# Kernel optimization log

Hardware: AMD Instinct MI355X
Metric: run time of the kernel (lower is better)

Reference implementation:

```python
import jax, jax.numpy as jnp
import numpy as np

N_DOCS = 1_000_000
N_FEAT = 136
BATCH = 1_000_000

# MSLR feature column indices used by the original module
COL_DOCLEN = 14      # metadata docLength
COL_WHOLE_LEN = 16   # used for avgDocLength statistic
COL_TF = 24          # term frequency feature
COL_INLINK = 127
COL_OUTLINK = 128
COL_PAGERANK = 129


def setup_inputs() -> dict:
    key = jax.random.key(0)
    k_feat, k_idx, kb, kpr, kin, kout = jax.random.split(key, 6)
    global_features = jax.random.uniform(k_feat, (N_DOCS, N_FEAT), dtype=jnp.float32)
    batch_indices = jax.random.randint(k_idx, (BATCH,), 0, N_DOCS)
    return {
        "batch_indices": batch_indices,
        "global_features": global_features,
        "k1": jnp.asarray(3.5, jnp.float32),
        "b": jnp.asarray(0.5, jnp.float32),
        "bm25_weight": jnp.asarray(1.0, jnp.float32),
        "page_rank": jnp.asarray(0.2, jnp.float32),
        "in_link": jnp.asarray(0.1, jnp.float32),
        "out_link": jnp.asarray(0.1, jnp.float32),
        "freshness": jnp.asarray(1.0, jnp.float32),
    }


def reference(batch_indices, global_features, k1, b, bm25_weight, page_rank,
              in_link, out_link, freshness):
    # Global doc statistics (computed once, like fetch_total_doc_statistics_mslr)
    avg_doc_len = jnp.mean(global_features[:, COL_WHOLE_LEN])
    total_docs = jnp.float32(global_features.shape[0])

    # Vectorized gather of per-doc features for the batch
    rows = global_features[batch_indices]            # [B, F]
    term_freq = rows[:, COL_TF]                      # [B]
    doc_length = rows[:, COL_DOCLEN]                 # [B]
    pr = rows[:, COL_PAGERANK]
    inl = rows[:, COL_INLINK]
    outl = rows[:, COL_OUTLINK]

    # In the original, num_docs_with_term == total corpus size (constant)
    num_docs_with_term = total_docs
    idf_term = jnp.log((total_docs - num_docs_with_term + 0.5) / (num_docs_with_term + 0.5) + 1.0)

    numerator = term_freq * (k1 + 1.0)
    denominator = term_freq + k1 * (1.0 - b + b * (doc_length / avg_doc_len))
    bm25_score = idf_term * (numerator / denominator)

    pagerank_score = page_rank * pr + in_link * inl + out_link * outl

    # torch.rand(1).item() per doc -> a random constant per doc, scaled by freshness
    fresh_noise = jax.random.uniform(jax.random.key(1), (batch_indices.shape[0],), dtype=jnp.float32)
    freshness_score = fresh_noise * freshness

    scores = bm25_weight * bm25_score + pagerank_score + freshness_score
    return scores[:, None]  # [B, 1]
```

## Files before the change

kernel.cpp:

```cpp
#include <hip/hip_runtime.h>
#include <hip/hip_bf16.h>
#include <stdint.h>

#define N_FEAT 136
#define COL_DOCLEN 14
#define COL_WHOLE_LEN 16
#define COL_TF 24
#define COL_INLINK 127
#define COL_OUTLINK 128
#define COL_PAGERANK 129

__device__ __forceinline__ void threefry2x32(uint32_t k0, uint32_t k1,
                                             uint32_t& x0, uint32_t& x1) {
  const uint32_t ks0 = k0, ks1 = k1, ks2 = k0 ^ k1 ^ 0x1BD11BDAu;
  x0 += ks0; x1 += ks1;
#define TF_ROUND(r) { x0 += x1; x1 = (x1 << (r)) | (x1 >> (32 - (r))); x1 ^= x0; }
  TF_ROUND(13) TF_ROUND(15) TF_ROUND(26) TF_ROUND(6)
  x0 += ks1; x1 += ks2 + 1u;
  TF_ROUND(17) TF_ROUND(29) TF_ROUND(16) TF_ROUND(24)
  x0 += ks2; x1 += ks0 + 2u;
  TF_ROUND(13) TF_ROUND(15) TF_ROUND(26) TF_ROUND(6)
  x0 += ks0; x1 += ks1 + 3u;
  TF_ROUND(17) TF_ROUND(29) TF_ROUND(16) TF_ROUND(24)
  x0 += ks1; x1 += ks2 + 4u;
  TF_ROUND(13) TF_ROUND(15) TF_ROUND(26) TF_ROUND(6)
  x0 += ks2; x1 += ks0 + 5u;
#undef TF_ROUND
}

__global__ void col16_sum_kernel(const float* __restrict__ gf, float* __restrict__ sum,
                                 int n_docs) {
  int stride = gridDim.x * blockDim.x;
  float v = 0.f;
  for (int j = blockIdx.x * blockDim.x + threadIdx.x; j < n_docs; j += stride)
    v += gf[(size_t)j * N_FEAT + COL_WHOLE_LEN];
  for (int off = 32; off > 0; off >>= 1) v += __shfl_down(v, off, 64);
  __shared__ float ws[4];
  int lane = threadIdx.x & 63, wave = threadIdx.x >> 6;
  if (lane == 0) ws[wave] = v;
  __syncthreads();
  if (threadIdx.x == 0) {
    float t = 0.f;
    int nw = blockDim.x >> 6;
    for (int w = 0; w < nw; ++w) t += ws[w];
    atomicAdd(sum, t);
  }
}

__global__ void score_kernel(const int* __restrict__ idx,
                             const float* __restrict__ gf,
                             const float* __restrict__ p_k1,
                             const float* __restrict__ p_b,
                             const float* __restrict__ p_bm25w,
                             const float* __restrict__ p_prw,
                             const float* __restrict__ p_inw,
                             const float* __restrict__ p_outw,
                             const float* __restrict__ p_fresh,
                             const float* __restrict__ col_sum,
                             float* __restrict__ out,
                             int batch, float total_docs) {
  int i = blockIdx.x * blockDim.x + threadIdx.x;
  if (i >= batch) return;

  const float k1 = p_k1[0];
  const float b  = p_b[0];
  const float bm25w = p_bm25w[0];
  const float prw   = p_prw[0];
  const float inw   = p_inw[0];
  const float outw  = p_outw[0];
  const float fresh = p_fresh[0];
  const float avg_doc_len = col_sum[0] / total_docs;

  const float idf = logf(0.5f / (total_docs + 0.5f) + 1.0f);

  const size_t base = (size_t)idx[i] * N_FEAT;
  const float tf   = gf[base + COL_TF];
  const float dl   = gf[base + COL_DOCLEN];
  const float pr   = gf[base + COL_PAGERANK];
  const float inl  = gf[base + COL_INLINK];
  const float outl = gf[base + COL_OUTLINK];

  const float numer = tf * (k1 + 1.0f);
  const float denom = tf + k1 * (1.0f - b + b * (dl / avg_doc_len));
  const float bm25 = idf * (numer / denom);

  uint32_t x0 = 0u, x1 = (uint32_t)i;
  threefry2x32(0u, 1u, x0, x1);
  const uint32_t bits = x0 ^ x1;
  const float noise = __uint_as_float((bits >> 9) | 0x3f800000u) - 1.0f;

  out[i] = bm25w * bm25 + prw * pr + inw * inl + outw * outl + noise * fresh;
}

extern "C" void kernel_launch(void* const* d_in, const int* in_sizes, int n_in,
                              void* d_out, int out_size, void* d_ws, size_t ws_size,
                              hipStream_t stream) {
  const int*   batch_indices = (const int*)d_in[0];
  const float* gf            = (const float*)d_in[1];
  const float* k1    = (const float*)d_in[2];
  const float* b     = (const float*)d_in[3];
  const float* bm25w = (const float*)d_in[4];
  const float* prw   = (const float*)d_in[5];
  const float* inw   = (const float*)d_in[6];
  const float* outw  = (const float*)d_in[7];
  const float* fresh = (const float*)d_in[8];
  float* out = (float*)d_out;
  float* col_sum = (float*)d_ws;

  const int batch  = in_sizes[0];
  const int n_docs = in_sizes[1] / N_FEAT;

  hipMemsetAsync(col_sum, 0, sizeof(float), stream);

  col16_sum_kernel<<<1024, 256, 0, stream>>>(gf, col_sum, n_docs);

  const int threads = 256;
  const int blocks = (batch + threads - 1) / threads;
  score_kernel<<<blocks, threads, 0, stream>>>(
      batch_indices, gf, k1, b, bm25w, prw, inw, outw, fresh,
      col_sum, out, batch, (float)n_docs);
}
```

Baseline: 664.0 us.

## Precompute per-doc scores in a sequential pass, then gather by index

Replaces the random-row gather of five feature columns with a sequential per-document pass. That pass extracts tf, doc length and the link score into compact arrays and computes the column-16 sum at the same time. A second kernel computes a per-document score, and a gather kernel reads one float per batch element with vectorized index loads and stores. The goal is to cut scattered cache-line fetches from the 544-byte rows, though it now touches every document instead of only the sampled ones. It needs workspace for four arrays and falls back to the old path otherwise.

```diff
diff --git a/kernel.cpp b/kernel.cpp
--- a/kernel.cpp
+++ b/kernel.cpp
@@ -1,5 +1,4 @@
 #include <hip/hip_runtime.h>
-#include <hip/hip_bf16.h>
 #include <stdint.h>
 
 #define N_FEAT 136
@@ -28,6 +27,88 @@
 #undef TF_ROUND
 }
 
+__device__ __forceinline__ float tf_noise(uint32_t i) {
+  uint32_t x0 = 0u, x1 = i;
+  threefry2x32(0u, 1u, x0, x1);
+  const uint32_t bits = x0 ^ x1;
+  return __uint_as_float((bits >> 9) | 0x3f800000u) - 1.0f;
+}
+
+__global__ void doc_pass_kernel(const float* __restrict__ gf,
+                                const float* __restrict__ p_prw,
+                                const float* __restrict__ p_inw,
+                                const float* __restrict__ p_outw,
+                                float* __restrict__ tf_a,
+                                float* __restrict__ dl_a,
+                                float* __restrict__ link_a,
+                                float* __restrict__ sum,
+                                int n_docs) {
+  const int j = blockIdx.x * blockDim.x + threadIdx.x;
+  float wl = 0.f;
+  if (j < n_docs) {
+    const size_t base = (size_t)j * N_FEAT;
+    const float dl  = gf[base + COL_DOCLEN];
+    wl              = gf[base + COL_WHOLE_LEN];
+    const float tf  = gf[base + COL_TF];
+    const float inl = gf[base + COL_INLINK];
+    const float2 op = *reinterpret_cast<const float2*>(gf + base + COL_OUTLINK);
+    tf_a[j]   = tf;
+    dl_a[j]   = dl;
+    link_a[j] = p_prw[0] * op.y + p_inw[0] * inl + p_outw[0] * op.x;
+  }
+  for (int off = 32; off > 0; off >>= 1) wl += __shfl_down(wl, off, 64);
+  __shared__ float ws_[4];
+  const int lane = threadIdx.x & 63, wave = threadIdx.x >> 6;
+  if (lane == 0) ws_[wave] = wl;
+  __syncthreads();
+  if (threadIdx.x == 0) atomicAdd(sum, ws_[0] + ws_[1] + ws_[2] + ws_[3]);
+}
+
+__global__ void doc_score_kernel(const float* __restrict__ tf_a,
+                                 const float* __restrict__ dl_a,
+                                 const float* __restrict__ link_a,
+                                 const float* __restrict__ p_k1,
+                                 const float* __restrict__ p_b,
+                                 const float* __restrict__ p_bm25w,
+                                 const float* __restrict__ col_sum,
+                                 float* __restrict__ s_doc,
+                                 int n_docs, float total_docs) {
+  const int j = blockIdx.x * blockDim.x + threadIdx.x;
+  if (j >= n_docs) return;
+  const float k1 = p_k1[0];
+  const float b  = p_b[0];
+  const float bm25w = p_bm25w[0];
+  const float avg_doc_len = col_sum[0] / total_docs;
+  const float idf = logf(0.5f / (total_docs + 0.5f) + 1.0f);
+  const float tf = tf_a[j];
+  const float dl = dl_a[j];
+  const float numer = tf * (k1 + 1.0f);
+  const float denom = tf + k1 * (1.0f - b + b * (dl / avg_doc_len));
+  const float bm25 = idf * (numer / denom);
+  s_doc[j] = bm25w * bm25 + link_a[j];
+}
+
+__global__ void gather_kernel(const int* __restrict__ idx,
+                              const float* __restrict__ s_doc,
+                              const float* __restrict__ p_fresh,
+                              float* __restrict__ out, int batch) {
+  const int t = blockIdx.x * blockDim.x + threadIdx.x;
+  int i = t * 4;
+  const float fresh = p_fresh[0];
+  if (i + 3 < batch) {
+    const int4 id = *reinterpret_cast<const int4*>(idx + i);
+    float4 r;
+    r.x = s_doc[id.x] + tf_noise((uint32_t)(i + 0)) * fresh;
+    r.y = s_doc[id.y] + tf_noise((uint32_t)(i + 1)) * fresh;
+    r.z = s_doc[id.z] + tf_noise((uint32_t)(i + 2)) * fresh;
+    r.w = s_doc[id.w] + tf_noise((uint32_t)(i + 3)) * fresh;
+    *reinterpret_cast<float4*>(out + i) = r;
+  } else {
+    for (; i < batch; ++i)
+      out[i] = s_doc[idx[i]] + tf_noise((uint32_t)i) * fresh;
+  }
+}
+
 __global__ void col16_sum_kernel(const float* __restrict__ gf, float* __restrict__ sum,
                                  int n_docs) {
   int stride = gridDim.x * blockDim.x;
@@ -61,35 +142,22 @@
                              int batch, float total_docs) {
   int i = blockIdx.x * blockDim.x + threadIdx.x;
   if (i >= batch) return;
-
   const float k1 = p_k1[0];
   const float b  = p_b[0];
   const float bm25w = p_bm25w[0];
-  const float prw   = p_prw[0];
-  const float inw   = p_inw[0];
-  const float outw  = p_outw[0];
-  const float fresh = p_fresh[0];
   const float avg_doc_len = col_sum[0] / total_docs;
-
   const float idf = logf(0.5f / (total_docs + 0.5f) + 1.0f);
-
   const size_t base = (size_t)idx[i] * N_FEAT;
   const float tf   = gf[base + COL_TF];
   const float dl   = gf[base + COL_DOCLEN];
   const float pr   = gf[base + COL_PAGERANK];
   const float inl  = gf[base + COL_INLINK];
   const float outl = gf[base + COL_OUTLINK];
-
   const float numer = tf * (k1 + 1.0f);
   const float denom = tf + k1 * (1.0f - b + b * (dl / avg_doc_len));
   const float bm25 = idf * (numer / denom);
-
-  uint32_t x0 = 0u, x1 = (uint32_t)i;
-  threefry2x32(0u, 1u, x0, x1);
-  const uint32_t bits = x0 ^ x1;
-  const float noise = __uint_as_float((bits >> 9) | 0x3f800000u) - 1.0f;
-
-  out[i] = bm25w * bm25 + prw * pr + inw * inl + outw * outl + noise * fresh;
+  out[i] = bm25w * bm25 + p_prw[0] * pr + p_inw[0] * inl + p_outw[0] * outl
+         + tf_noise((uint32_t)i) * p_fresh[0];
 }
 
 extern "C" void kernel_launch(void* const* d_in, const int* in_sizes, int n_in,
@@ -105,18 +173,34 @@
   const float* outw  = (const float*)d_in[7];
   const float* fresh = (const float*)d_in[8];
   float* out = (float*)d_out;
-  float* col_sum = (float*)d_ws;
 
   const int batch  = in_sizes[0];
   const int n_docs = in_sizes[1] / N_FEAT;
 
+  float* ws      = (float*)d_ws;
+  float* col_sum = ws;
+  float* tf_a    = ws + 64;
+  float* dl_a    = tf_a + n_docs;
+  float* link_a  = dl_a + n_docs;
+  float* s_doc   = link_a + n_docs;
+  const size_t need = (64 + 4 * (size_t)n_docs) * sizeof(float);
+
   hipMemsetAsync(col_sum, 0, sizeof(float), stream);
 
-  col16_sum_kernel<<<1024, 256, 0, stream>>>(gf, col_sum, n_docs);
-
-  const int threads = 256;
-  const int blocks = (batch + threads - 1) / threads;
-  score_kernel<<<blocks, threads, 0, stream>>>(
-      batch_indices, gf, k1, b, bm25w, prw, inw, outw, fresh,
-      col_sum, out, batch, (float)n_docs);
-}
+  const int tpb = 256;
+  if (ws_size >= need) {
+    const int b_doc = (n_docs + tpb - 1) / tpb;
+    doc_pass_kernel<<<b_doc, tpb, 0, stream>>>(gf, prw, inw, outw,
+                                               tf_a, dl_a, link_a, col_sum, n_docs);
+    doc_score_kernel<<<b_doc, tpb, 0, stream>>>(tf_a, dl_a, link_a, k1, b, bm25w,
+                                                col_sum, s_doc, n_docs, (float)n_docs);
+    const int b_gat = ((batch + 3) / 4 + tpb - 1) / tpb;
+    gather_kernel<<<b_gat, tpb, 0, stream>>>(batch_indices, s_doc, fresh, out, batch);
+  } else {
+    col16_sum_kernel<<<1024, tpb, 0, stream>>>(gf, col_sum, n_docs);
+    const int blocks = (batch + tpb - 1) / tpb;
+    score_kernel<<<blocks, tpb, 0, stream>>>(
+        batch_indices, gf, k1, b, bm25w, prw, inw, outw, fresh,
+        col_sum, out, batch, (float)n_docs);
+  }
+}
```

Measured after the change: 674.3 us. About the same (+1.5%).
